# Optimization experiments

Measured on AMD Instinct MI355X. Metric: run time of the kernel, lower is better.

## Reference

```python
import jax, jax.numpy as jnp
import numpy as np

K0 = 0.7978845608028654  # sqrt(2/pi)
C1 = 0.044715

def _gelu_tanh(x):
    # tanh-approx GELU, matching the Triton kernel's math
    return 0.5 * x * (1.0 + jnp.tanh(K0 * (x + C1 * x * x * x)))

def setup_inputs() -> dict:
    key = jax.random.key(0)
    k1, k2, k3 = jax.random.split(key, 3)
    B, C_in, H, W = 32, 64, 128, 128
    C_out, KH = 128, 3
    x = jax.random.normal(k1, (B, C_in, H, W), dtype=jnp.float32)
    weight = jax.random.normal(k2, (C_out, C_in, KH, KH), dtype=jnp.float32)
    bias = jax.random.normal(k3, (C_out,), dtype=jnp.float32)
    return {"x": x, "weight": weight, "bias": bias}

def reference(x, weight, bias):
    # Valid conv2d, stride 1 (NCHW, OIHW)
    y = jax.lax.conv_general_dilated(
        x, weight,
        window_strides=(1, 1), padding="VALID",
        dimension_numbers=("NCHW", "OIHW", "NCHW"))
    y = y + bias[None, :, None, None]
    y = _gelu_tanh(y)
    # global average pool over spatial dims -> [B, C_out]
    return jnp.mean(y, axis=(2, 3))
```

## Files before the change

### kernel.cpp

```cpp
#include <hip/hip_runtime.h>
#include <cstdint>
#include <cstddef>

#define GK0 0.7978845608028654f
#define GC1 0.044715f

typedef __attribute__((ext_vector_type(8))) short short8;
typedef __attribute__((ext_vector_type(4))) float floatx4;

__device__ __forceinline__ unsigned short f2bf(float f) {
  union { float f; unsigned int u; } v; v.f = f;
  unsigned int r = v.u + 0x7fffu + ((v.u >> 16) & 1u);
  return (unsigned short)(r >> 16);
}

__device__ __forceinline__ void gl_lds16(const unsigned short* g, unsigned short* l) {
  __builtin_amdgcn_global_load_lds(
      (const __attribute__((address_space(1))) unsigned int*)g,
      (__attribute__((address_space(3))) unsigned int*)l, 16, 0, 0);
}

__global__ void k_wt(const float* __restrict__ w, unsigned short* __restrict__ wt,
                     float* __restrict__ out) {
  if (blockIdx.x == 0) {
    for (int i = threadIdx.x; i < 32 * 128; i += 256) out[i] = 0.0f;
  }
  int t = blockIdx.x * 256 + threadIdx.x;
  if (t >= 128 * 64 * 9) return;
  int co = t / 576; int r = t - co * 576; int ci = r / 9; int khw = r - ci * 9;
  wt[(khw * 128 + co) * 64 + ci] = f2bf(w[t]);
}

__global__ __launch_bounds__(256) void k_xt(const float* __restrict__ x,
                                            unsigned short* __restrict__ xb) {
  __shared__ float tile[64 * 132];
  const int tid = threadIdx.x, lane = tid & 63, wv = tid >> 6;
  const int b = blockIdx.y, h0 = blockIdx.x * 4;
  const int w4 = lane & 31, cih = lane >> 5;

  for (int r = 0; r < 4; r++) {
    const int h = h0 + r;
#pragma unroll
    for (int j = 0; j < 8; j++) {
      const int ci = wv * 16 + 2 * j + cih;
      float4 f = *(const float4*)(x + ((size_t)(b * 64 + ci) * 128 + h) * 128 + 4 * w4);
      *(float4*)&tile[ci * 132 + 4 * w4] = f;
    }
    __syncthreads();
    unsigned short* orow = xb + ((size_t)b * 128 + h) * 8192;
    const int oct = tid & 7, wlo = tid >> 3;
#pragma unroll
    for (int it = 0; it < 4; it++) {
      const int w = wlo + 32 * it;
      short8 v;
#pragma unroll
      for (int j = 0; j < 8; j++) v[j] = (short)f2bf(tile[(8 * oct + j) * 132 + w]);
      *(short8*)(orow + w * 64 + oct * 8) = v;
    }
    __syncthreads();
  }
}

__global__ __launch_bounds__(256, 3) void k_conv(
    const unsigned short* __restrict__ xb, const unsigned short* __restrict__ wt,
    const float* __restrict__ bias, float* __restrict__ out) {
  __shared__ __align__(16) unsigned short As[8192];
  __shared__ __align__(16) unsigned short Bs[8192];
  const int tid = threadIdx.x, lane = tid & 63, wv = tid >> 6;
  const int w0 = blockIdx.x * 64, h0 = blockIdx.y * 2, b = blockIdx.z;
  const int wm = wv & 1, wn = wv >> 1;
  const int m = lane & 15, q = lane >> 4;

  floatx4 acc[4][4];
#pragma unroll
  for (int i = 0; i < 4; i++)
#pragma unroll
    for (int j = 0; j < 4; j++) acc[i][j] = (floatx4){0.f, 0.f, 0.f, 0.f};

  const unsigned short* xbb = xb + (size_t)b * 128 * 8192;
  const int rh = wv >> 1, cc0 = (wv & 1) * 4;

#pragma unroll
  for (int khw = 0; khw < 9; khw++) {
    const int kh = khw / 3, kw = khw - 3 * kh;
    const unsigned short* ag = wt + khw * 8192 + wv * 2048 + lane * 8;
    unsigned short* al = As + wv * 2048;
#pragma unroll
    for (int i = 0; i < 4; i++) gl_lds16(ag + i * 512, al + i * 512);
    const unsigned short* bg =
        xbb + ((size_t)(h0 + rh + kh) * 128 + w0 + kw) * 64 + cc0 * 512 + lane * 8;
    unsigned short* bl = Bs + (rh * 8 + cc0) * 512;
#pragma unroll
    for (int i = 0; i < 4; i++) gl_lds16(bg + i * 512, bl + i * 512);
    __syncthreads();

#pragma unroll
    for (int half = 0; half < 2; half++) {
      short8 a[4], bf[4];
#pragma unroll
      for (int mt = 0; mt < 4; mt++)
        a[mt] = *(const short8*)&As[(wm * 64 + mt * 16 + m) * 64 + half * 32 + q * 8];
#pragma unroll
      for (int nt = 0; nt < 4; nt++)
        bf[nt] = *(const short8*)&Bs[(wn * 64 + nt * 16 + m) * 64 + half * 32 + q * 8];
#pragma unroll
      for (int mt = 0; mt < 4; mt++)
#pragma unroll
        for (int nt = 0; nt < 4; nt++)
          acc[mt][nt] = __builtin_amdgcn_mfma_f32_16x16x32_bf16(a[mt], bf[nt], acc[mt][nt], 0, 0, 0);
    }
    __syncthreads();
  }

  const float inv_area = 1.0f / (126.0f * 126.0f);
  float* orow = out + b * 128;
#pragma unroll
  for (int mt = 0; mt < 4; mt++)
#pragma unroll
    for (int r2 = 0; r2 < 4; r2++) {
      const int co = wm * 64 + mt * 16 + q * 4 + r2;
      const float bv = bias[co];
      float s = 0.f;
#pragma unroll
      for (int nt = 0; nt < 4; nt++) {
        float y = acc[mt][nt][r2] + bv;
        float u = GK0 * (y + GC1 * y * y * y);
        float e = __expf(-2.0f * u);
        float g = y * __builtin_amdgcn_rcpf(1.0f + e);
        if (w0 + nt * 16 + m < 126) s += g;
      }
#pragma unroll
      for (int d = 1; d < 16; d <<= 1) s += __shfl_xor(s, d, 64);
      if (m == 0) atomicAdd(&orow[co], s * inv_area);
    }
}

extern "C" void kernel_launch(void* const* d_in, const int* in_sizes, int n_in,
                              void* d_out, int out_size, void* d_ws, size_t ws_size,
                              hipStream_t stream) {
  const float* x    = (const float*)d_in[0];
  const float* w    = (const float*)d_in[1];
  const float* bias = (const float*)d_in[2];
  float* out = (float*)d_out;

  const size_t xb_elems = (size_t)32 * 128 * 8192;
  unsigned short* xbuf = (unsigned short*)d_ws;
  unsigned short* wbuf = xbuf + xb_elems + 2048;
  if (ws_size < xb_elems * 2 + 4096 + (size_t)9 * 128 * 64 * 2) return;

  k_wt<<<288, 256, 0, stream>>>(w, wbuf, out);
  k_xt<<<dim3(32, 32), 256, 0, stream>>>(x, xbuf);
  k_conv<<<dim3(2, 63, 32), 256, 0, stream>>>(xbuf, wbuf, bias, out);
}
```

Before: 378.3 us.

## Reuse input row across kw shifts, double-buffer rows, read weights from global

The conv kernel now stages one 72-pixel input row per output row into LDS, double-buffered across kh, and reuses it for all three kw shifts instead of reloading a shifted tile for each of the nine taps. Weight fragments are read directly from global/L2 rather than staged through LDS, and the LDS layout is XOR-swizzled to avoid bank conflicts. The transpose kernel now handles one row per block with a swizzled tile, and k_conv's occupancy hint drops to 2 blocks per CU. The change cuts LDS traffic and barriers, but weight loads now go through global memory and the kernel may run at lower occupancy.

New measurement: 427.9 us. 13.1% more time.

```diff
diff --git a/kernel.cpp b/kernel.cpp
--- a/kernel.cpp
+++ b/kernel.cpp
@@ -35,41 +35,41 @@
                                             unsigned short* __restrict__ xb) {
   __shared__ float tile[64 * 132];
   const int tid = threadIdx.x, lane = tid & 63, wv = tid >> 6;
-  const int b = blockIdx.y, h0 = blockIdx.x * 4;
+  const int b = blockIdx.y, h = blockIdx.x;
   const int w4 = lane & 31, cih = lane >> 5;
 
-  for (int r = 0; r < 4; r++) {
-    const int h = h0 + r;
+#pragma unroll
+  for (int j = 0; j < 8; j++) {
+    const int ci = wv * 16 + 2 * j + cih;
+    float4 f = *(const float4*)(x + ((size_t)(b * 64 + ci) * 128 + h) * 128 + 4 * w4);
+    *(float4*)((char*)tile + ci * 528 + ((16 * w4) ^ (((ci >> 3) & 7) << 4))) = f;
+  }
+  __syncthreads();
+  unsigned short* orow = xb + ((size_t)b * 128 + h) * 8192;
+  const int oct = tid & 7, wlo = tid >> 3;
+#pragma unroll
+  for (int it = 0; it < 4; it++) {
+    const int w = wlo + 32 * it;
+    short8 v;
 #pragma unroll
     for (int j = 0; j < 8; j++) {
-      const int ci = wv * 16 + 2 * j + cih;
-      float4 f = *(const float4*)(x + ((size_t)(b * 64 + ci) * 128 + h) * 128 + 4 * w4);
-      *(float4*)&tile[ci * 132 + 4 * w4] = f;
+      const float f =
+          *(const float*)((const char*)tile + (8 * oct + j) * 528 + ((4 * w) ^ (oct << 4)));
+      v[j] = (short)f2bf(f);
     }
-    __syncthreads();
-    unsigned short* orow = xb + ((size_t)b * 128 + h) * 8192;
-    const int oct = tid & 7, wlo = tid >> 3;
-#pragma unroll
-    for (int it = 0; it < 4; it++) {
-      const int w = wlo + 32 * it;
-      short8 v;
-#pragma unroll
-      for (int j = 0; j < 8; j++) v[j] = (short)f2bf(tile[(8 * oct + j) * 132 + w]);
-      *(short8*)(orow + w * 64 + oct * 8) = v;
-    }
-    __syncthreads();
+    *(short8*)(orow + w * 64 + oct * 8) = v;
   }
 }
 
-__global__ __launch_bounds__(256, 3) void k_conv(
+__global__ __launch_bounds__(256, 2) void k_conv(
     const unsigned short* __restrict__ xb, const unsigned short* __restrict__ wt,
     const float* __restrict__ bias, float* __restrict__ out) {
-  __shared__ __align__(16) unsigned short As[8192];
-  __shared__ __align__(16) unsigned short Bs[8192];
+  __shared__ __align__(16) unsigned short Bs[2][9216];
   const int tid = threadIdx.x, lane = tid & 63, wv = tid >> 6;
   const int w0 = blockIdx.x * 64, h0 = blockIdx.y * 2, b = blockIdx.z;
   const int wm = wv & 1, wn = wv >> 1;
   const int m = lane & 15, q = lane >> 4;
+  const int swz = ((lane >> 3) << 6) + (((lane & 7) ^ (lane >> 3)) << 3);
 
   floatx4 acc[4][4];
 #pragma unroll
@@ -78,36 +78,44 @@
     for (int j = 0; j < 4; j++) acc[i][j] = (floatx4){0.f, 0.f, 0.f, 0.f};
 
   const unsigned short* xbb = xb + (size_t)b * 128 * 8192;
-  const int rh = wv >> 1, cc0 = (wv & 1) * 4;
+
+  auto stage = [&](unsigned short* bs, int row0) {
+    for (int c = wv; c < 18; c += 4) {
+      const int rh = (c >= 9) ? 1 : 0;
+      const int j = c - 9 * rh;
+      gl_lds16(xbb + ((size_t)((row0 + rh) * 128 + w0) << 6) + j * 512 + swz,
+               bs + rh * 4608 + j * 512);
+    }
+  };
+
+  stage(Bs[0], h0);
+  __syncthreads();
 
 #pragma unroll
-  for (int khw = 0; khw < 9; khw++) {
-    const int kh = khw / 3, kw = khw - 3 * kh;
-    const unsigned short* ag = wt + khw * 8192 + wv * 2048 + lane * 8;
-    unsigned short* al = As + wv * 2048;
+  for (int kh = 0; kh < 3; kh++) {
+    if (kh < 2) stage(Bs[(kh + 1) & 1], h0 + kh + 1);
+    const unsigned short* bsr = Bs[kh & 1] + wn * 4608;
 #pragma unroll
-    for (int i = 0; i < 4; i++) gl_lds16(ag + i * 512, al + i * 512);
-    const unsigned short* bg =
-        xbb + ((size_t)(h0 + rh + kh) * 128 + w0 + kw) * 64 + cc0 * 512 + lane * 8;
-    unsigned short* bl = Bs + (rh * 8 + cc0) * 512;
+    for (int kw = 0; kw < 3; kw++) {
+      const int khw = kh * 3 + kw;
+      const int xr = ((m + kw) & 7) << 3;
 #pragma unroll
-    for (int i = 0; i < 4; i++) gl_lds16(bg + i * 512, bl + i * 512);
-    __syncthreads();
-
+      for (int half = 0; half < 2; half++) {
+        const int colb = half * 32 + q * 8;
+        short8 a[4], bf[4];
 #pragma unroll
-    for (int half = 0; half < 2; half++) {
-      short8 a[4], bf[4];
-#pragma unroll
-      for (int mt = 0; mt < 4; mt++)
-        a[mt] = *(const short8*)&As[(wm * 64 + mt * 16 + m) * 64 + half * 32 + q * 8];
-#pragma unroll
-      for (int nt = 0; nt < 4; nt++)
-        bf[nt] = *(const short8*)&Bs[(wn * 64 + nt * 16 + m) * 64 + half * 32 + q * 8];
-#pragma unroll
-      for (int mt = 0; mt < 4; mt++)
+        for (int mt = 0; mt < 4; mt++)
+          a[mt] = *(const short8*)(wt + khw * 8192 + (wm * 64 + mt * 16 + m) * 64 + colb);
 #pragma unroll
         for (int nt = 0; nt < 4; nt++)
-          acc[mt][nt] = __builtin_amdgcn_mfma_f32_16x16x32_bf16(a[mt], bf[nt], acc[mt][nt], 0, 0, 0);
+          bf[nt] = *(const short8*)(bsr + (nt * 16 + m + kw) * 64 + (colb ^ xr));
+#pragma unroll
+        for (int mt = 0; mt < 4; mt++)
+#pragma unroll
+          for (int nt = 0; nt < 4; nt++)
+            acc[mt][nt] =
+                __builtin_amdgcn_mfma_f32_16x16x32_bf16(a[mt], bf[nt], acc[mt][nt], 0, 0, 0);
+      }
     }
     __syncthreads();
   }
@@ -149,6 +157,6 @@
   if (ws_size < xb_elems * 2 + 4096 + (size_t)9 * 128 * 64 * 2) return;
 
   k_wt<<<288, 256, 0, stream>>>(w, wbuf, out);
-  k_xt<<<dim3(32, 32), 256, 0, stream>>>(x, xbuf);
+  k_xt<<<dim3(128, 32), 256, 0, stream>>>(x, xbuf);
   k_conv<<<dim3(2, 63, 32), 256, 0, stream>>>(xbuf, wbuf, bias, out);
 }
```
